# Kernel optimization log

Measured on AMD Instinct MI355X. Metric: run time of the kernel, lower is better.

Reference implementation:

```python
import jax, jax.numpy as jnp
import numpy as np

E = 100000   # n_entities
R = 64       # n_relations
I = 256      # in_channels
O = 256      # out_channels
N_EDGES = 1_600_000


def setup_inputs() -> dict:
    key = jax.random.key(0)
    k1, k2, k3, k4 = jax.random.split(key, 4)
    x = jax.random.normal(k1, (E, I), dtype=jnp.float32)
    # cs must be nonzero (it is reciprocated); uniform in [0.5, 1.5)
    cs = jax.random.uniform(k2, (E, R), dtype=jnp.float32) + 0.5
    W = jax.random.normal(k3, (R, I, O), dtype=jnp.float32) * 0.05
    edge_index = jax.random.randint(k4, (2, N_EDGES), 0, E, dtype=jnp.int64)
    return {"x": x, "cs": cs, "W": W, "edge_index": edge_index}


def reference(x, cs, W, edge_index):
    # Faithful to: torch.einsum('er,rio,ej->eo', 1/cs, W, x)
    # i and j are independently contracted indices, so this factorizes:
    # out[e,o] = (sum_j x[e,j]) * sum_r (1/cs[e,r]) * (sum_i W[r,i,o])
    cs_reciprocal = 1.0 / cs                 # (E, R)
    W_sum = jnp.sum(W, axis=1)               # (R, O)
    x_sum = jnp.sum(x, axis=1)               # (E,)
    src = (cs_reciprocal @ W_sum) * x_sum[:, None]  # (E, O)
    return src
```

## Files before the change

kernel.cpp:

```cpp
#include <hip/hip_runtime.h>


constexpr int En = 100000;
constexpr int Rn = 64;
constexpr int In = 256;
constexpr int On = 256;
constexpr int TILES = En / 16;

typedef short bf16x8 __attribute__((ext_vector_type(8)));
typedef float floatx4 __attribute__((ext_vector_type(4)));

static __device__ __forceinline__ short f2bf(float f) {
    unsigned u = __builtin_bit_cast(unsigned, f);
    unsigned r = (u + 0x7FFFu + ((u >> 16) & 1u)) >> 16;
    return (short)r;
}

__global__ __launch_bounds__(1024) void wsum_kernel(const float* __restrict__ W,
                                                    short* __restrict__ wsumT) {
    __shared__ float red[16][65];
    const int r  = blockIdx.x >> 2;
    const int h  = blockIdx.x & 3;
    const int ol = threadIdx.x & 63;
    const int ic = threadIdx.x >> 6;
    const int o  = h * 64 + ol;
    const float* base = W + ((size_t)r * In + (size_t)ic * 16) * On + o;
    float s = 0.f;
#pragma unroll
    for (int i = 0; i < 16; ++i) s += base[(size_t)i * On];
    red[ic][ol] = s;
    __syncthreads();
    if (ic == 0) {
        float t = 0.f;
#pragma unroll
        for (int j = 0; j < 16; ++j) t += red[j][ol];
        wsumT[o * Rn + r] = f2bf(t);
    }
}

__global__ __launch_bounds__(256) void xsum_kernel(const float* __restrict__ x,
                                                   float* __restrict__ xsum,
                                                   int xstride) {
    const int w    = (blockIdx.x * 256 + (int)threadIdx.x) >> 6;
    const int nw   = (gridDim.x * 256) >> 6;
    const int lane = threadIdx.x & 63;
    for (int base = w * 4; base < En; base += nw * 4) {
        float s[4];
#pragma unroll
        for (int u = 0; u < 4; ++u) {
            const int row = base + u;
            float4 v = make_float4(0.f, 0.f, 0.f, 0.f);
            if (row < En)
                v = *(const float4*)&x[(size_t)row * In + lane * 4];
            s[u] = (v.x + v.y) + (v.z + v.w);
        }
#pragma unroll
        for (int u = 0; u < 4; ++u) {
#pragma unroll
            for (int off = 32; off; off >>= 1) s[u] += __shfl_down(s[u], off, 64);
        }
        if (lane == 0) {
#pragma unroll
            for (int u = 0; u < 4; ++u)
                if (base + u < En) xsum[(size_t)(base + u) * xstride] = s[u];
        }
    }
}

__global__ __launch_bounds__(256) void out_kernel(const float* __restrict__ cs,
                                                  const short* __restrict__ wsumT,
                                                  const float* __restrict__ xsum,
                                                  int xstride,
                                                  float* __restrict__ out) {
    const int gw = (blockIdx.x * 256 + (int)threadIdx.x) >> 6;
    const int nw = (gridDim.x * 256) >> 6;
    const int ln = threadIdx.x & 63;
    const int lm = ln & 15;
    const int q  = ln >> 4;

    bf16x8 wa0[16], wa1[16];
#pragma unroll
    for (int ot = 0; ot < 16; ++ot) {
        const short* p = wsumT + ((ot * 16 + lm) * Rn + q * 8);
        wa0[ot] = *(const bf16x8*)p;
        wa1[ot] = *(const bf16x8*)(p + 32);
    }

    int t = gw;
    if (t >= TILES) return;
    float4 c0, c1, c2, c3;
    float xv;
    {
        const float* p = cs + (size_t)(t * 16 + lm) * Rn + q * 8;
        c0 = *(const float4*)p;        c1 = *(const float4*)(p + 4);
        c2 = *(const float4*)(p + 32); c3 = *(const float4*)(p + 36);
        xv = xsum[(size_t)(t * 16 + lm) * xstride];
    }
    while (true) {
        const int tn = t + nw;
        const float4 d0 = c0, d1 = c1, d2 = c2, d3 = c3;
        const float xs = xv;
        if (tn < TILES) {
            const float* p = cs + (size_t)(tn * 16 + lm) * Rn + q * 8;
            c0 = *(const float4*)p;        c1 = *(const float4*)(p + 4);
            c2 = *(const float4*)(p + 32); c3 = *(const float4*)(p + 36);
            xv = xsum[(size_t)(tn * 16 + lm) * xstride];
        }
        bf16x8 b0, b1;
        {
            const float rv[16] = {d0.x, d0.y, d0.z, d0.w, d1.x, d1.y, d1.z, d1.w,
                                  d2.x, d2.y, d2.z, d2.w, d3.x, d3.y, d3.z, d3.w};
#pragma unroll
            for (int j = 0; j < 8; ++j) {
                b0[j] = f2bf(__builtin_amdgcn_rcpf(rv[j]));
                b1[j] = f2bf(__builtin_amdgcn_rcpf(rv[8 + j]));
            }
        }
        float* orow = out + (size_t)(t * 16 + lm) * On + q * 4;
#pragma unroll
        for (int ot = 0; ot < 16; ++ot) {
            floatx4 acc = {0.f, 0.f, 0.f, 0.f};
            acc = __builtin_amdgcn_mfma_f32_16x16x32_bf16(wa0[ot], b0, acc, 0, 0, 0);
            acc = __builtin_amdgcn_mfma_f32_16x16x32_bf16(wa1[ot], b1, acc, 0, 0, 0);
            const float4 st = make_float4(acc[0] * xs, acc[1] * xs,
                                          acc[2] * xs, acc[3] * xs);
            *(float4*)(orow + ot * 16) = st;
        }
        if (tn >= TILES) break;
        t = tn;
    }
}

extern "C" void kernel_launch(void* const* d_in, const int* in_sizes, int n_in,
                              void* d_out, int out_size, void* d_ws, size_t ws_size,
                              hipStream_t stream) {
    const float* x  = (const float*)d_in[0];
    const float* cs = (const float*)d_in[1];
    const float* W  = (const float*)d_in[2];
    float* out = (float*)d_out;

    short* wsumT = (short*)d_ws;
    float* xsum;
    int xstride;
    if (ws_size >= (size_t)(32768 + En * 4)) {
        xsum = (float*)((char*)d_ws + 32768);
        xstride = 1;
    } else {
        xsum = out;
        xstride = On;
    }

    wsum_kernel<<<dim3(256), dim3(1024), 0, stream>>>(W, wsumT);
    xsum_kernel<<<dim3(2048), dim3(256), 0, stream>>>(x, xsum, xstride);
    out_kernel<<<dim3(512), dim3(256), 0, stream>>>(cs, wsumT, xsum, xstride, out);
}
```

Measured before the change: 231.2 us.

## Fuse x row-sum into output MFMA kernel and stage W-sum in LDS

Merges the separate xsum kernel into the output kernel, so each wave reads its x rows directly and reduces them with shuffles. This removes one launch and the xsum write and readback. The bf16 W-sum operands move from per-wave registers into shared memory, loaded once per block. Work is statically assigned as two tiles per wave across 782 blocks, replacing the grid-stride loop with software prefetch. Loads and stores use nontemporal hints. In exchange the cs prefetch overlap is lost and the MFMA operands are reread from LDS for every tile.

```diff
diff --git a/kernel.cpp b/kernel.cpp
--- a/kernel.cpp
+++ b/kernel.cpp
@@ -5,15 +5,16 @@
 constexpr int Rn = 64;
 constexpr int In = 256;
 constexpr int On = 256;
-constexpr int TILES = En / 16;
+constexpr int TILES  = En / 16;
+constexpr int BLOCKS = 782;
+constexpr int WAVES  = TILES / 2;
 
 typedef short bf16x8 __attribute__((ext_vector_type(8)));
 typedef float floatx4 __attribute__((ext_vector_type(4)));
 
 static __device__ __forceinline__ short f2bf(float f) {
     unsigned u = __builtin_bit_cast(unsigned, f);
-    unsigned r = (u + 0x7FFFu + ((u >> 16) & 1u)) >> 16;
-    return (short)r;
+    return (short)((u + 0x7FFFu + ((u >> 16) & 1u)) >> 16);
 }
 
 __global__ __launch_bounds__(1024) void wsum_kernel(const float* __restrict__ W,
@@ -38,96 +39,78 @@
     }
 }
 
-__global__ __launch_bounds__(256) void xsum_kernel(const float* __restrict__ x,
-                                                   float* __restrict__ xsum,
-                                                   int xstride) {
-    const int w    = (blockIdx.x * 256 + (int)threadIdx.x) >> 6;
-    const int nw   = (gridDim.x * 256) >> 6;
-    const int lane = threadIdx.x & 63;
-    for (int base = w * 4; base < En; base += nw * 4) {
-        float s[4];
+__global__ __launch_bounds__(256) void fused_kernel(const float* __restrict__ x,
+                                                    const float* __restrict__ cs,
+                                                    const short* __restrict__ wsumT,
+                                                    float* __restrict__ out) {
+    __shared__ floatx4 Wf[2048];
+
+    const int t = threadIdx.x;
+    {
+        const floatx4* wq = (const floatx4*)wsumT;
 #pragma unroll
-        for (int u = 0; u < 4; ++u) {
-            const int row = base + u;
-            float4 v = make_float4(0.f, 0.f, 0.f, 0.f);
-            if (row < En)
-                v = *(const float4*)&x[(size_t)row * In + lane * 4];
-            s[u] = (v.x + v.y) + (v.z + v.w);
-        }
-#pragma unroll
-        for (int u = 0; u < 4; ++u) {
-#pragma unroll
-            for (int off = 32; off; off >>= 1) s[u] += __shfl_down(s[u], off, 64);
-        }
-        if (lane == 0) {
-#pragma unroll
-            for (int u = 0; u < 4; ++u)
-                if (base + u < En) xsum[(size_t)(base + u) * xstride] = s[u];
+        for (int k = 0; k < 8; ++k) {
+            const int e    = t + 256 * k;
+            const int half = e >> 10;
+            const int idx  = e & 1023;
+            const int ot   = idx >> 6;
+            const int q    = (idx >> 4) & 3;
+            const int lm   = idx & 15;
+            Wf[e] = wq[(ot * 16 + lm) * 8 + half * 4 + q];
         }
     }
-}
+    __syncthreads();
 
-__global__ __launch_bounds__(256) void out_kernel(const float* __restrict__ cs,
-                                                  const short* __restrict__ wsumT,
-                                                  const float* __restrict__ xsum,
-                                                  int xstride,
-                                                  float* __restrict__ out) {
-    const int gw = (blockIdx.x * 256 + (int)threadIdx.x) >> 6;
-    const int nw = (gridDim.x * 256) >> 6;
-    const int ln = threadIdx.x & 63;
+    const int ln = t & 63;
     const int lm = ln & 15;
     const int q  = ln >> 4;
+    const int v  = (t >> 6) * BLOCKS + blockIdx.x;
+    if (v >= WAVES) return;
 
-    bf16x8 wa0[16], wa1[16];
+    const bf16x8* WfA = (const bf16x8*)Wf;
+
 #pragma unroll
-    for (int ot = 0; ot < 16; ++ot) {
-        const short* p = wsumT + ((ot * 16 + lm) * Rn + q * 8);
-        wa0[ot] = *(const bf16x8*)p;
-        wa1[ot] = *(const bf16x8*)(p + 32);
-    }
+    for (int pass = 0; pass < 2; ++pass) {
+        const int tl = v + pass * WAVES;
+        const size_t e = (size_t)tl * 16 + lm;
 
-    int t = gw;
-    if (t >= TILES) return;
-    float4 c0, c1, c2, c3;
-    float xv;
-    {
-        const float* p = cs + (size_t)(t * 16 + lm) * Rn + q * 8;
-        c0 = *(const float4*)p;        c1 = *(const float4*)(p + 4);
-        c2 = *(const float4*)(p + 32); c3 = *(const float4*)(p + 36);
-        xv = xsum[(size_t)(t * 16 + lm) * xstride];
-    }
-    while (true) {
-        const int tn = t + nw;
-        const float4 d0 = c0, d1 = c1, d2 = c2, d3 = c3;
-        const float xs = xv;
-        if (tn < TILES) {
-            const float* p = cs + (size_t)(tn * 16 + lm) * Rn + q * 8;
-            c0 = *(const float4*)p;        c1 = *(const float4*)(p + 4);
-            c2 = *(const float4*)(p + 32); c3 = *(const float4*)(p + 36);
-            xv = xsum[(size_t)(tn * 16 + lm) * xstride];
-        }
+        const floatx4* pc = (const floatx4*)(cs + e * Rn) + q * 2;
+        const floatx4 c0 = __builtin_nontemporal_load(pc);
+        const floatx4 c1 = __builtin_nontemporal_load(pc + 1);
+        const floatx4 c2 = __builtin_nontemporal_load(pc + 8);
+        const floatx4 c3 = __builtin_nontemporal_load(pc + 9);
+
+        const floatx4* px = (const floatx4*)(x + e * In) + q * 16;
+        floatx4 sx = {0.f, 0.f, 0.f, 0.f};
+#pragma unroll
+        for (int j = 0; j < 16; ++j)
+            sx += __builtin_nontemporal_load(px + j);
+        float s = (sx[0] + sx[1]) + (sx[2] + sx[3]);
+        s += __shfl_xor(s, 16, 64);
+        s += __shfl_xor(s, 32, 64);
+
         bf16x8 b0, b1;
         {
-            const float rv[16] = {d0.x, d0.y, d0.z, d0.w, d1.x, d1.y, d1.z, d1.w,
-                                  d2.x, d2.y, d2.z, d2.w, d3.x, d3.y, d3.z, d3.w};
+            const float rv[16] = {c0[0], c0[1], c0[2], c0[3], c1[0], c1[1], c1[2], c1[3],
+                                  c2[0], c2[1], c2[2], c2[3], c3[0], c3[1], c3[2], c3[3]};
 #pragma unroll
             for (int j = 0; j < 8; ++j) {
                 b0[j] = f2bf(__builtin_amdgcn_rcpf(rv[j]));
                 b1[j] = f2bf(__builtin_amdgcn_rcpf(rv[8 + j]));
             }
         }
-        float* orow = out + (size_t)(t * 16 + lm) * On + q * 4;
+
+        float* orow = out + e * On + q * 4;
 #pragma unroll
         for (int ot = 0; ot < 16; ++ot) {
+            const bf16x8 wa0 = WfA[ot * 64 + ln];
+            const bf16x8 wa1 = WfA[1024 + ot * 64 + ln];
             floatx4 acc = {0.f, 0.f, 0.f, 0.f};
-            acc = __builtin_amdgcn_mfma_f32_16x16x32_bf16(wa0[ot], b0, acc, 0, 0, 0);
-            acc = __builtin_amdgcn_mfma_f32_16x16x32_bf16(wa1[ot], b1, acc, 0, 0, 0);
-            const float4 st = make_float4(acc[0] * xs, acc[1] * xs,
-                                          acc[2] * xs, acc[3] * xs);
-            *(float4*)(orow + ot * 16) = st;
+            acc = __builtin_amdgcn_mfma_f32_16x16x32_bf16(wa0, b0, acc, 0, 0, 0);
+            acc = __builtin_amdgcn_mfma_f32_16x16x32_bf16(wa1, b1, acc, 0, 0, 0);
+            const floatx4 st = acc * s;
+            __builtin_nontemporal_store(st, (floatx4*)(orow + ot * 16));
         }
-        if (tn >= TILES) break;
-        t = tn;
     }
 }
 
@@ -137,20 +120,9 @@
     const float* x  = (const float*)d_in[0];
     const float* cs = (const float*)d_in[1];
     const float* W  = (const float*)d_in[2];
-    float* out = (float*)d_out;
-
+    float* out   = (float*)d_out;
     short* wsumT = (short*)d_ws;
-    float* xsum;
-    int xstride;
-    if (ws_size >= (size_t)(32768 + En * 4)) {
-        xsum = (float*)((char*)d_ws + 32768);
-        xstride = 1;
-    } else {
-        xsum = out;
-        xstride = On;
-    }
 
     wsum_kernel<<<dim3(256), dim3(1024), 0, stream>>>(W, wsumT);
-    xsum_kernel<<<dim3(2048), dim3(256), 0, stream>>>(x, xsum, xstride);
-    out_kernel<<<dim3(512), dim3(256), 0, stream>>>(cs, wsumT, xsum, xstride, out);
+    fused_kernel<<<dim3(BLOCKS), dim3(256), 0, stream>>>(x, cs, wsumT, out);
 }
```

Result: slower. 277.2 us (+19.9%).
